# Optimization experiments

Hardware: AMD Instinct MI355X
Metric: run time of the kernel (lower is better)

Reference implementation:

```python
import jax, jax.numpy as jnp
import numpy as np

B, S, T1, V = 32, 60, 60, 50000   # batch, post len, response len (decoder runs T1-1 steps), vocab
E, A, H, ATT, DI = 300, 300, 512, 512, 512  # word emb, affect emb, rnn hidden, attention size, decoder input


def setup_inputs() -> dict:
    key = jax.random.key(0)
    ks = jax.random.split(key, 20)
    p = lambda i, shape: jax.random.normal(ks[i], shape, jnp.float32) * 0.02
    z = lambda n: jnp.zeros((n,), jnp.float32)
    return {
        'posts': jax.random.randint(ks[0], (B, S), 0, V),
        'responses': jax.random.randint(ks[1], (B, T1), 0, V),
        'len_posts': jnp.full((B,), S, jnp.int32),
        'emb': p(2, (V, E)), 'affect_emb': p(3, (V, A)),
        'enc_Wi': p(4, (3 * H, E)), 'enc_Wh': p(5, (3 * H, H)), 'enc_bi': z(3 * H), 'enc_bh': z(3 * H),
        'aff_Wi': p(6, (3 * H, A)), 'aff_Wh': p(7, (3 * H, H)), 'aff_bi': z(3 * H), 'aff_bh': z(3 * H),
        'Wp': p(8, (H, 2 * H)), 'bp': z(H),
        'Wl': p(9, (DI, E + H + ATT)), 'bl': z(DI),
        'dec_Wi': p(10, (3 * H, DI)), 'dec_Wh': p(11, (3 * H, H)), 'dec_bi': z(3 * H), 'dec_bh': z(3 * H),
        'Wa': p(12, (H, H)), 'Wc': p(13, (ATT, H)), 'bc': z(ATT),
        'Wv': p(14, (V, H + ATT)), 'bv': z(V),
    }


def _gru_cell(x, h, Wi, Wh, bi, bh):
    gi = x @ Wi.T + bi
    gh = h @ Wh.T + bh
    ir, iz, inn = jnp.split(gi, 3, -1)
    hr, hz, hn = jnp.split(gh, 3, -1)
    r = jax.nn.sigmoid(ir + hr)
    zg = jax.nn.sigmoid(iz + hz)
    n = jnp.tanh(inn + r * hn)
    return (1.0 - zg) * n + zg * h


def _gru_seq(xs, h0, Wi, Wh, bi, bh):
    # xs: [S, B, in] -> (outputs [S,B,H], h_last [B,H])
    def step(h, x):
        h2 = _gru_cell(x, h, Wi, Wh, bi, bh)
        return h2, h2
    hT, ys = jax.lax.scan(step, h0, xs)
    return ys, hT


def reference(posts, responses, len_posts, emb, affect_emb,
              enc_Wi, enc_Wh, enc_bi, enc_bh,
              aff_Wi, aff_Wh, aff_bi, aff_bh,
              Wp, bp, Wl, bl,
              dec_Wi, dec_Wh, dec_bi, dec_bh,
              Wa, Wc, bc, Wv, bv):
    embed_posts = emb[posts]            # [B,S,E]
    affect_posts = affect_emb[posts]    # [B,S,A]
    h0 = jnp.zeros((posts.shape[0], H), embed_posts.dtype)

    _, state_encoder = _gru_seq(embed_posts.transpose(1, 0, 2), h0, enc_Wi, enc_Wh, enc_bi, enc_bh)
    out_affect, state_affect = _gru_seq(affect_posts.transpose(1, 0, 2), h0, aff_Wi, aff_Wh, aff_bi, aff_bh)
    context_affect = out_affect[-1]     # [B,H] (all lengths == S)
    K = out_affect.transpose(1, 0, 2)   # [B,S,H] attention keys/values

    # PrepareState: Linear + tanh on concat of both encoder final states
    state0 = jnp.tanh(jnp.concatenate([state_encoder, state_affect], -1) @ Wp.T + bp)

    dec_in = emb[responses[:, :-1]].transpose(1, 0, 2)  # [T,B,E]
    init_attn = jnp.zeros((posts.shape[0], ATT), embed_posts.dtype)

    def dec_step(carry, x_emb):
        h, attn = carry
        x = jnp.concatenate([x_emb, context_affect, attn], -1) @ Wl.T + bl
        h = _gru_cell(x, h, dec_Wi, dec_Wh, dec_bi, dec_bh)
        scores = jnp.einsum('bd,bsd->bs', h @ Wa, K)        # Luong 'general'
        w = jax.nn.softmax(scores, -1)
        ctx = jnp.einsum('bs,bsd->bd', w, K)
        attn = jnp.tanh(ctx @ Wc.T + bc)
        return (h, attn), (jnp.concatenate([h, attn], -1), w)

    _, (outs, weights) = jax.lax.scan(dec_step, (state0, init_attn), dec_in)
    outs = outs.transpose(1, 0, 2)          # [B,T,H+ATT]
    weights = weights.transpose(1, 0, 2)    # [B,T,S]
    output_vocab = jax.nn.softmax(outs @ Wv.T + bv, -1)  # [B,T,V]
    return output_vocab, weights
```

## Files before the change

### kernel.cpp

```cpp
#include <hip/hip_runtime.h>

typedef unsigned int uint32;
typedef unsigned short u16;
typedef unsigned long long u64;
typedef __attribute__((ext_vector_type(8))) short bf8;
typedef __attribute__((ext_vector_type(4))) float f4;
typedef __attribute__((ext_vector_type(4))) uint32 u32x4;

#define DEV static __device__ __forceinline__

DEV f4 MFMA(bf8 a, bf8 b, f4 c) {
  return __builtin_amdgcn_mfma_f32_16x16x32_bf16(a, b, c, 0, 0, 0);
}
DEV u16 f2bf(float f) {
  uint32 u = __float_as_uint(f);
  return (u16)((u + 0x7FFFu + ((u >> 16) & 1u)) >> 16);
}
DEV float bf2f(u16 h) { return __uint_as_float(((uint32)h) << 16); }
DEV float bfLO(uint32 u) { return __uint_as_float(u << 16); }
DEV float bfHI(uint32 u) { return __uint_as_float(u & 0xFFFF0000u); }
DEV float sigmoid_(float x) { return 1.f / (1.f + __expf(-x)); }
DEV float tanh_(float x) {
  float cx = fminf(fmaxf(x, -15.f), 15.f);
  float e = __expf(2.f * cx);
  return (e - 1.f) / (e + 1.f);
}

DEV u64 ldA64(const void* p) {
  return __hip_atomic_load((u64*)p, __ATOMIC_RELAXED, __HIP_MEMORY_SCOPE_AGENT);
}
DEV void stA64(void* p, u64 v) {
  __hip_atomic_store((u64*)p, v, __ATOMIC_RELAXED, __HIP_MEMORY_SCOPE_AGENT);
}
DEV void stA32(int* p, int v) {
  __hip_atomic_store(p, v, __ATOMIC_RELAXED, __HIP_MEMORY_SCOPE_AGENT);
}
DEV bf8 pk_frag(u64 lo, u64 hi) {
  u32x4 v = {(uint32)lo, (uint32)(lo >> 32), (uint32)hi, (uint32)(hi >> 32)};
  return __builtin_bit_cast(bf8, v);
}

DEV void wait_vm0() { asm volatile("s_waitcnt vmcnt(0)" ::: "memory"); }
DEV void wait_slots(const int* slots, int n, int tgt) {
  const int lane = threadIdx.x & 63;
  for (int i = 0; i < (1 << 20); ++i) {
    int v = 0x7fffffff;
    if (lane < n)
      v = __hip_atomic_load((int*)(slots + lane), __ATOMIC_RELAXED,
                            __HIP_MEMORY_SCOPE_AGENT);
    if (__all(v >= tgt)) return;
    __builtin_amdgcn_s_sleep(1);
  }
}

namespace L {
constexpr size_t o_flags  = 0;
constexpr size_t o_rowsum = 4096;
constexpr size_t o_bcomb  = 11776;
constexpr size_t o_gistat = 17920;
constexpr size_t o_xbuf   = 214528;
constexpr size_t o_henc   = 345600;
constexpr size_t o_haff   = 411136;
constexpr size_t o_cat    = 476672;
constexpr size_t o_Kbuf   = 542208;
constexpr size_t o_KA     = 2508288;
constexpr size_t o_embP   = 4474368;
constexpr size_t o_embA   = 5703168;
constexpr size_t o_embD   = 6931968;
constexpr size_t o_encWi  = 8140288;
constexpr size_t o_affWi  = 9123328;
constexpr size_t o_Whe    = 10106368;
constexpr size_t o_Wha    = 11679232;
constexpr size_t o_decWi  = 13252096;
constexpr size_t o_WlT    = 14824960;
constexpr size_t o_Wa     = 16184832;
constexpr size_t o_Wp     = 16709120;
constexpr size_t o_wq     = 17757696;
constexpr size_t o_Wcomb  = 18281984;
constexpr size_t o_WdE    = 26441216;
constexpr size_t o_WdA    = 27424256;
constexpr size_t o_Wd2    = 28997120;
constexpr size_t o_giE    = 32142848;
constexpr size_t o_giA    = 43939328;
constexpr size_t o_giD    = 55735808;
constexpr size_t o_outsB  = 67335680;
constexpr size_t o_WvB    = 71267840;
constexpr size_t WS_FULL  = 174028288;
constexpr size_t WOFF = 94400000;
}

__global__ __launch_bounds__(256) void kp_gather(
    const int* __restrict__ posts, const int* __restrict__ resp,
    const float* __restrict__ emb, const float* __restrict__ aemb, char* ws)
{
  using namespace L;
  const int gid = blockIdx.x * 256 + threadIdx.x;
  const int r = gid / 320, e = gid - r * 320;
  u16* embP = (u16*)(ws + o_embP);
// ... 33 lines not shown
  gid -= 983040;
  if (gid < 2359296) {
    const int g = (int)(gid / 786432);
    const long u = gid - (long)g * 786432;
    const float* src = g == 0 ? encWh : (g == 1 ? affWh : dWi);
    u16* dst = (u16*)(ws + (g == 0 ? o_Whe : (g == 1 ? o_Wha : o_decWi)));
    dst[u] = f2bf(src[u]);
    return;
  }
  gid -= 2359296;
  if (gid < 679936) {
    const int j = (int)(gid >> 9), k = (int)(gid & 511);
    ((u16*)(ws + o_WlT))[gid] = f2bf(j < 1324 ? Wl[(size_t)k * 1324 + j] : 0.f);
    return;
  }
  gid -= 679936;
  if (gid < 262144) { ((u16*)(ws + o_Wa))[gid] = f2bf(Wa[gid]); return; }
  gid -= 262144;
  if (gid < 524288) { ((u16*)(ws + o_Wp))[gid] = f2bf(Wp[gid]); return; }
  gid -= 524288;
  if (gid < 131072) {
    const int q = (int)(gid & 3), j = (int)((gid >> 2) & 511), g4 = (int)(gid >> 11);
    const int d0 = g4 * 8 + q * 2;
    const uint32 lo = f2bf(Wc[(size_t)j * 512 + d0]);
    const uint32 hi = f2bf(Wc[(size_t)j * 512 + d0 + 1]);
    ((uint32*)(ws + o_wq))[gid] = lo | (hi << 16);
    return;
  }
  gid -= 131072;
  if (gid < 2944) {
    if (gid < 1024) ((uint32*)(ws + o_flags))[gid] = 0;
    else ((uint32*)(ws + o_rowsum))[gid - 1024] = 0;
    return;
  }
  gid -= 2944;
  if (gid < 49152) {
    if (gid < 16384) ((uint32*)(ws + o_outsB + (size_t)1888 * 1024 * 2))[gid] = 0;
    else if (gid < 32768) ((uint32*)(ws + o_henc))[gid - 16384] = 0;
    else ((uint32*)(ws + o_haff))[gid - 32768] = 0;
  }
}

__global__ __launch_bounds__(256) void kp_bcomb(
    const float* __restrict__ dWi, const float* __restrict__ bl,
    const float* __restrict__ dbi, char* ws)
{
  const int i = blockIdx.x * 256 + threadIdx.x;
  if (i >= 1536) return;
  float a = dbi[i];
  for (int k = 0; k < 512; ++k) a += dWi[(size_t)i * 512 + k] * bl[k];
  ((float*)(ws + L::o_bcomb))[i] = a;
}

__global__ __launch_bounds__(256) void kp_wv(const float* __restrict__ Wv, char* ws)
{
  const long gid = (long)blockIdx.x * 256 + threadIdx.x;
  const int r = (int)(gid >> 8), q = (int)(gid & 255);
  u16* WvB = (u16*)(ws + L::o_WvB);
  uint2 o;
  if (r < 50000) {
    const float4 f = *(const float4*)(Wv + (size_t)r * 1024 + q * 4);
    o.x = (uint32)f2bf(f.x) | ((uint32)f2bf(f.y) << 16);
    o.y = (uint32)f2bf(f.z) | ((uint32)f2bf(f.w) << 16);
  } else { o.x = 0u; o.y = 0u; }
  *(uint2*)(WvB + (size_t)r * 1024 + q * 4) = o;
}

__global__ __launch_bounds__(256) void kp_pack2(
    const float* __restrict__ Wcomb, const float* __restrict__ dWh, char* ws)
{
  using namespace L;
  long gid = (long)blockIdx.x * 256 + threadIdx.x;
  if (gid < 491520) {
    const int n = (int)(gid / 320), e = (int)(gid - (long)n * 320);
    ((u16*)(ws + o_WdE))[gid] = f2bf(e < 300 ? Wcomb[(size_t)n * 1328 + e] : 0.f);
    return;
  }
  gid -= 491520;
  if (gid < 786432) {
    const int n = (int)(gid >> 9), k = (int)(gid & 511);
    ((u16*)(ws + o_WdA))[gid] = f2bf(Wcomb[(size_t)n * 1328 + 300 + k]);
    return;
  }
  gid -= 786432;
  if (gid < 1572864) {
    const int n = (int)(gid >> 10), k = (int)(gid & 1023);
    const float v = (k < 512) ? Wcomb[(size_t)n * 1328 + 812 + k]
                              : dWh[(size_t)n * 512 + (k - 512)];
    ((u16*)(ws + o_Wd2))[gid] = f2bf(v);
  }
}

__global__ __launch_bounds__(256) void k_gemm_nt(
    const u16* __restrict__ A, const u16* __restrict__ Bm,
    float* __restrict__ C, const float* __restrict__ bias,
    const int M, const int N, const int Kp)
{
  const int mt = blockIdx.x, cb = blockIdx.y;
  const int w = threadIdx.x >> 6, lane = threadIdx.x & 63;
  const int l15 = lane & 15, lhi = lane >> 4;
  const u16* arow = A + (size_t)(mt * 16 + l15) * Kp + lhi * 8;
  const int c0 = cb * 256 + w * 64;
  f4 acc[4];
#pragma unroll
  for (int nn = 0; nn < 4; ++nn) acc[nn] = (f4){0.f, 0.f, 0.f, 0.f};
  for (int k = 0; k < Kp; k += 32) {
    const bf8 a = *(const bf8*)(arow + k);
#pragma unroll
    for (int nn = 0; nn < 4; ++nn) {
      const int cs = c0 + nn * 16;
      if (cs < N) {
        const bf8 b = *(const bf8*)(Bm + (size_t)(cs + l15) * Kp + k + lhi * 8);
        acc[nn] = MFMA(a, b, acc[nn]);
      }
    }
  }
#pragma unroll
  for (int nn = 0; nn < 4; ++nn) {
    const int cs = c0 + nn * 16;
    if (cs >= N) continue;
    const int c = cs + l15;
    const float bb = bias ? bias[c] : 0.f;
#pragma unroll
    for (int j = 0; j < 4; ++j) {
      const int r = mt * 16 + lhi * 4 + j;
      C[(size_t)r * N + c] = acc[nn][j] + bb;
    }
  }
}

__global__ __launch_bounds__(256, 1) void k_enc(
    char* __restrict__ ws, const float* __restrict__ enc_bh,
    const float* __restrict__ aff_bh)
{
  using namespace L;
  const int tid = threadIdx.x, blk = blockIdx.x;
  const int wave = tid >> 6, lane = tid & 63;
  const int l15 = lane & 15, lhi = lane >> 4;
  const int g = blk >> 5;
  const bool act = wave < 2;
  int* flags = (int*)(ws + o_flags);
  int* slotE = flags + 128 + g * 64;
  const u16* Wh = (const u16*)(ws + (g ? o_Wha : o_Whe));
  const float* gi = (const float*)(ws + (g ? o_giA : o_giE));
  const float* bh = g ? aff_bh : enc_bh;
  u16* hbuf = (u16*)(ws + (g ? o_haff : o_henc));
  u16* cat = (u16*)(ws + o_cat);
  u16* Kb = (u16*)(ws + o_Kbuf);

  const int wid = (blk & 31) * 2 + (wave & 1);
  const int btile = wid >> 5, ctile = wid & 31;
  const int bl = btile * 16 + l15;
  const int c0 = ctile * 16 + lhi * 4;
  const u16* wr0 = Wh + (size_t)(ctile * 16 + l15) * 512 + lhi * 8;
  const u16* wr1 = wr0 + (size_t)512 * 512;
  const u16* wr2 = wr1 + (size_t)512 * 512;
  f4 bhr4 = {0.f, 0.f, 0.f, 0.f}, bhz4 = bhr4, bhn4 = bhr4;
  if (act) {
    bhr4 = *(const f4*)(bh + c0);
    bhz4 = *(const f4*)(bh + 512 + c0);
    bhn4 = *(const f4*)(bh + 1024 + c0);
  }
  for (int s = 0; s < 60; ++s) {
    const u16* hin = hbuf + (s & 1) * (32 * 512);
    u16* hout = hbuf + ((s & 1) ^ 1) * (32 * 512);
    if (act) {
      const u16* brow = hin + bl * 512 + lhi * 8;
      u64 flo[16], fhi[16];
#pragma unroll
      for (int kk = 0; kk < 16; ++kk) {
        flo[kk] = ldA64(brow + kk * 32);
        fhi[kk] = ldA64(brow + kk * 32 + 4);
      }
      const u64 hq = ldA64(hin + bl * 512 + c0);
      f4 ar = {0.f, 0.f, 0.f, 0.f}, az = ar, an = ar;
#pragma unroll
      for (int kk = 0; kk < 16; ++kk) {
        const bf8 hf = pk_frag(flo[kk], fhi[kk]);
        ar = MFMA(*(const bf8*)(wr0 + kk * 32), hf, ar);
        az = MFMA(*(const bf8*)(wr1 + kk * 32), hf, az);
        an = MFMA(*(const bf8*)(wr2 + kk * 32), hf, an);
      }
      const float* gr = gi + (size_t)(s * 32 + bl) * 1536;
      const f4 g0 = *(const f4*)(gr + c0);
      const f4 g1 = *(const f4*)(gr + 512 + c0);
      const f4 g2 = *(const f4*)(gr + 1024 + c0);
      u64 pk = 0;
#pragma unroll
      for (int j = 0; j < 4; ++j) {
        const float r = sigmoid_(g0[j] + ar[j] + bhr4[j]);
        const float z = sigmoid_(g1[j] + az[j] + bhz4[j]);
        const float n = tanh_(g2[j] + r * (an[j] + bhn4[j]));
        const float hold = bf2f((u16)(hq >> (16 * j)));
        pk |= (u64)f2bf((1.f - z) * n + z * hold) << (16 * j);
      }
      stA64(hout + bl * 512 + c0, pk);
      if (g) *(u64*)(Kb + (size_t)(s * 32 + bl) * 512 + c0) = pk;
      if (s == 59) *(u64*)(cat + bl * 1024 + g * 512 + c0) = pk;
    }
    wait_vm0();
    __syncthreads();
    if (tid == 0) stA32(&slotE[blk & 31], s + 1);
    if (wave == 2) wait_slots(slotE, 32, s + 1);
    __syncthreads();
  }
}

__global__ __launch_bounds__(256) void k_mid(char* __restrict__ ws,
                                             const float* __restrict__ bp)
{
  using namespace L;
  const int tid = threadIdx.x, blk = blockIdx.x;
  const int wave = tid >> 6, lane = tid & 63;
  const int l15 = lane & 15, lhi = lane >> 4;
  u16* xb = (u16*)(ws + o_xbuf);
  u16* cat = (u16*)(ws + o_cat);
  u16* Kb = (u16*)(ws + o_Kbuf);

  if (blk < 16) {
    const u16* Wp_ = (const u16*)(ws + o_Wp);
    const int wid = blk * 4 + wave;
    const int btile = wid >> 5, ctile = wid & 31;
    const int bl = btile * 16 + l15;
    const int c0 = ctile * 16 + lhi * 4;
    const u16* arow = Wp_ + (size_t)(ctile * 16 + l15) * 1024 + lhi * 8;
    const u16* brow = cat + bl * 1024 + lhi * 8;
    f4 acc = {0.f, 0.f, 0.f, 0.f};
    for (int k = 0; k < 1024; k += 32)
      acc = MFMA(*(const bf8*)(arow + k), *(const bf8*)(brow + k), acc);
    const f4 bp4 = *(const f4*)(bp + c0);
    u64 pk = 0;
#pragma unroll
    for (int j = 0; j < 4; ++j)
      pk |= (u64)f2bf(tanh_(acc[j] + bp4[j])) << (16 * j);
    *(u64*)(xb + bl * 1024 + 512 + c0) = pk;
    *(u64*)(xb + bl * 1024 + c0) = 0;
  } else if (blk < 32) {
    const u16* WdA = (const u16*)(ws + o_WdA);
    const float* bco = (const float*)(ws + o_bcomb);
    float* gst = (float*)(ws + o_gistat);
    const int wid = (blk - 16) * 4 + wave;
    const int btile = wid >> 5, ctb = wid & 31;
    const int bl = btile * 16 + l15;
    const int c0 = ctb * 16 + lhi * 4;
    const u16* brow = cat + bl * 1024 + 512 + lhi * 8;
    const u16* a0p = WdA + (size_t)(ctb * 16 + l15) * 512 + lhi * 8;
    const u16* a1p = a0p + (size_t)512 * 512;
    const u16* a2p = a1p + (size_t)512 * 512;
    f4 a0 = {0.f, 0.f, 0.f, 0.f}, a1 = a0, a2 = a0;
    for (int k = 0; k < 512; k += 32) {
      const bf8 bfr = *(const bf8*)(brow + k);
      a0 = MFMA(*(const bf8*)(a0p + k), bfr, a0);
      a1 = MFMA(*(const bf8*)(a1p + k), bfr, a1);
      a2 = MFMA(*(const bf8*)(a2p + k), bfr, a2);
    }
    const f4 v0 = *(const f4*)(bco + c0);
    const f4 v1 = *(const f4*)(bco + 512 + c0);
    const f4 v2 = *(const f4*)(bco + 1024 + c0);
    *(f4*)(gst + bl * 1536 + c0) = a0 + v0;
    *(f4*)(gst + bl * 1536 + 512 + c0) = a1 + v1;
    *(f4*)(gst + bl * 1536 + 1024 + c0) = a2 + v2;
  } else {
    const u16* Wa_ = (const u16*)(ws + o_Wa);
    u16* KAp = (u16*)(ws + o_KA);
    const int widK = (blk - 32) * 4 + wave;
    for (int task = widK; task < 3840; task += 192) {
      const int mt = task >> 5, ct = task & 31;
      const int m = mt * 16 + l15;
      const int c0 = ct * 16 + lhi * 4;
      const u16* arow = Wa_ + (size_t)(ct * 16 + l15) * 512 + lhi * 8;
      const u16* brow = Kb + (size_t)m * 512 + lhi * 8;
      f4 acc = {0.f, 0.f, 0.f, 0.f};
      for (int k = 0; k < 512; k += 32)
        acc = MFMA(*(const bf8*)(arow + k), *(const bf8*)(brow + k), acc);
      u64 pk = 0;
#pragma unroll
      for (int j = 0; j < 4; ++j) pk |= (u64)f2bf(acc[j]) << (16 * j);
      *(u64*)(KAp + (size_t)m * 512 + c0) = pk;
    }
  }
}

__global__ __launch_bounds__(256, 1) void k_dec(
    char* __restrict__ ws, float* __restrict__ out,
    const float* __restrict__ dec_bh, const float* __restrict__ bc)
{
  using namespace L;
  const int tid = threadIdx.x, blk = blockIdx.x;
  const int wave = tid >> 6, lane = tid & 63;
  const int l15 = lane & 15, lhi = lane >> 4;
  int* flags = (int*)(ws + o_flags);
  int* slotA = flags;
  int* slotB = flags + 64;

  __shared__ float hsm[512];
  __shared__ float ctxs[512];
  __shared__ float scb[64];
  __shared__ float wsb[64];
  __shared__ u16 attn_sm[256];

  u16* xb = (u16*)(ws + o_xbuf);
  u16* outs = (u16*)(ws + o_outsB);

  if (blk < 32) {
    const bool act = wave < 2;
    const u16* Wd2 = (const u16*)(ws + o_Wd2);
    const float* gst = (const float*)(ws + o_gistat);
    const float* gD = (const float*)(ws + o_giD);
    const int wid = (blk & 31) * 2 + (wave & 1);
    const int btile = wid >> 5, ctile = wid & 31;
    const int bl = btile * 16 + l15;
    const int c0 = ctile * 16 + lhi * 4;
    const u16* wr = Wd2 + (size_t)(ctile * 16 + l15) * 1024 + lhi * 8;
    const u16* wz = wr + (size_t)512 * 1024;
    const u16* wn = wz + (size_t)512 * 1024;
    f4 bhr4 = {0.f, 0.f, 0.f, 0.f}, bhz4 = bhr4, bhn4 = bhr4;
    f4 s0 = bhr4, s1 = bhr4, s2 = bhr4;
    if (act) {
      bhr4 = *(const f4*)(dec_bh + c0);
      bhz4 = *(const f4*)(dec_bh + 512 + c0);
      bhn4 = *(const f4*)(dec_bh + 1024 + c0);
      s0 = *(const f4*)(gst + bl * 1536 + c0);
      s1 = *(const f4*)(gst + bl * 1536 + 512 + c0);
      s2 = *(const f4*)(gst + bl * 1536 + 1024 + c0);
    }
    for (int t = 0; t < 59; ++t) {
      const u16* xin = xb + (t & 1) * (32 * 1024);
      u16* xout = xb + ((t & 1) ^ 1) * (32 * 1024);
      const u16* brow = xin + bl * 1024 + lhi * 8;
      f4 ar = {0.f, 0.f, 0.f, 0.f}, az = ar, anx = ar, anh = ar;
      u64 hq = 0;
      f4 d0 = ar, d1 = ar, d2 = ar;
      if (t) {
        if (wave == 2) wait_slots(slotA, 32, t);
        __syncthreads();
      }
      if (act) {
        u64 flo[16], fhi[16];
#pragma unroll
        for (int kk = 0; kk < 16; ++kk) {
          flo[kk] = ldA64(brow + (16 + kk) * 32);
          fhi[kk] = ldA64(brow + (16 + kk) * 32 + 4);
        }
        hq = ldA64(xin + bl * 1024 + 512 + c0);
        const float* g2p = gD + (size_t)(t * 32 + bl) * 1536;
        d0 = *(const f4*)(g2p + c0);
        d1 = *(const f4*)(g2p + 512 + c0);
        d2 = *(const f4*)(g2p + 1024 + c0);
#pragma unroll
        for (int kk = 0; kk < 16; ++kk) {
          const bf8 xf = pk_frag(flo[kk], fhi[kk]);
          ar = MFMA(*(const bf8*)(wr + (16 + kk) * 32), xf, ar);
          az = MFMA(*(const bf8*)(wz + (16 + kk) * 32), xf, az);
          anh = MFMA(*(const bf8*)(wn + (16 + kk) * 32), xf, anh);
        }
      }
      if (t) {
        if (wave == 2) wait_slots(slotB, 64, t);
        __syncthreads();
      }
      if (act) {
        u64 glo[16], ghi[16];
#pragma unroll
        for (int kk = 0; kk < 16; ++kk) {
          glo[kk] = ldA64(brow + kk * 32);
          ghi[kk] = ldA64(brow + kk * 32 + 4);
        }
#pragma unroll
        for (int kk = 0; kk < 16; ++kk) {
          const bf8 xf = pk_frag(glo[kk], ghi[kk]);
          ar = MFMA(*(const bf8*)(wr + kk * 32), xf, ar);
          az = MFMA(*(const bf8*)(wz + kk * 32), xf, az);
          anx = MFMA(*(const bf8*)(wn + kk * 32), xf, anx);
        }
        u64 pk = 0;
#pragma unroll
        for (int j = 0; j < 4; ++j) {
          const float r = sigmoid_(s0[j] + d0[j] + ar[j] + bhr4[j]);
          const float z = sigmoid_(s1[j] + d1[j] + az[j] + bhz4[j]);
          const float n = tanh_(s2[j] + d2[j] + anx[j] + r * (anh[j] + bhn4[j]));
          const float hold = bf2f((u16)(hq >> (16 * j)));
          pk |= (u64)f2bf((1.f - z) * n + z * hold) << (16 * j);
        }
        stA64(xout + bl * 1024 + 512 + c0, pk);
        *(u64*)(outs + (size_t)(bl * 59 + t) * 1024 + c0) = pk;
      }
      wait_vm0();
      __syncthreads();
      if (tid == 0) stA32(&slotA[blk], t + 1);
    }
  } else {
    const int idx = blk - 32;
    const int b = idx >> 1, half = idx & 1;
    const u16* KAp = (const u16*)(ws + o_KA);
    const u16* Kb = (const u16*)(ws + o_Kbuf);
    const uint4* wq = (const uint4*)(ws + o_wq);
    for (int t = 0; t < 59; ++t) {
      if (wave == 0) wait_slots(slotA, 32, t + 1);
      __syncthreads();
      const u16* xcur = xb + ((t & 1) ^ 1) * (32 * 1024);
      if (tid < 128) {
        const u64 hv = ldA64(xcur + b * 1024 + 512 + tid * 4);
        const uint32 w0 = (uint32)hv, w1 = (uint32)(hv >> 32);
        hsm[tid * 4 + 0] = bfLO(w0);
        hsm[tid * 4 + 1] = bfHI(w0);
        hsm[tid * 4 + 2] = bfLO(w1);
        hsm[tid * 4 + 3] = bfHI(w1);
      }
      __syncthreads();
      if (tid < 240) {
        const int s = tid >> 2, q = tid & 3;
        const u16* kr = KAp + (size_t)(s * 32 + b) * 512 + q * 128;
        const float* hq = &hsm[q * 128];
        float acc0 = 0.f, acc1 = 0.f;
#pragma unroll 4
        for (int i = 0; i < 128; i += 8) {
          const uint2 k4 = *(const uint2*)(kr + i);
          const uint2 k5 = *(const uint2*)(kr + i + 4);
          const float4 h4 = *(const float4*)(hq + i);
          const float4 h5 = *(const float4*)(hq + i + 4);
          acc0 += h4.x * bfLO(k4.x) + h4.y * bfHI(k4.x)
                + h4.z * bfLO(k4.y) + h4.w * bfHI(k4.y);
          acc1 += h5.x * bfLO(k5.x) + h5.y * bfHI(k5.x)
                + h5.z * bfLO(k5.y) + h5.w * bfHI(k5.y);
        }
        float acc = acc0 + acc1;
        acc += __shfl_xor(acc, 1);
        acc += __shfl_xor(acc, 2);
        if ((tid & 3) == 0) scb[s] = acc;
      }
      __syncthreads();
      if (tid < 64) {
        const float v = (tid < 60) ? scb[tid] : -1e30f;
        float m = v;
#pragma unroll
        for (int d = 1; d < 64; d <<= 1) m = fmaxf(m, __shfl_xor(m, d));
        const float e = (tid < 60) ? __expf(v - m) : 0.f;
        float sm = e;
#pragma unroll
        for (int d = 1; d < 64; d <<= 1) sm += __shfl_xor(sm, d);
        const float w = e / sm;
        if (tid < 60) {
          wsb[tid] = w;
          if (half == 0) out[WOFF + (size_t)(b * 59 + t) * 60 + tid] = w;
        }
      }
      __syncthreads();
      {
        float c0a = 0.f, c0b = 0.f, c1a = 0.f, c1b = 0.f;
#pragma unroll 2
        for (int s = 0; s < 60; s += 2) {
          const float w0 = wsb[s], w1 = wsb[s + 1];
          const u16* kr0 = Kb + (size_t)(s * 32 + b) * 512;
          const u16* kr1 = Kb + (size_t)((s + 1) * 32 + b) * 512;
          c0a += w0 * bf2f(kr0[tid]);
          c1a += w0 * bf2f(kr0[tid + 256]);
          c0b += w1 * bf2f(kr1[tid]);
          c1b += w1 * bf2f(kr1[tid + 256]);
        }
        ctxs[tid] = c0a + c0b;
        ctxs[tid + 256] = c1a + c1b;
      }
      __syncthreads();
      const int jj = half * 256 + tid;
      float faa[4] = {0.f, 0.f, 0.f, 0.f};
      float fbb[4] = {0.f, 0.f, 0.f, 0.f};
#pragma unroll 4
      for (int g4 = 0; g4 < 64; ++g4) {
        const uint4 wv4 = wq[g4 * 512 + jj];
        const float4 ca = *(const float4*)&ctxs[g4 * 8];
        const float4 cb2 = *(const float4*)&ctxs[g4 * 8 + 4];
        faa[g4 & 3] += ca.x * bfLO(wv4.x) + ca.y * bfHI(wv4.x)
                     + ca.z * bfLO(wv4.y) + ca.w * bfHI(wv4.y);
        fbb[g4 & 3] += cb2.x * bfLO(wv4.z) + cb2.y * bfHI(wv4.z)
                     + cb2.z * bfLO(wv4.w) + cb2.w * bfHI(wv4.w);
      }
      const float fa = bc[jj] + faa[0] + faa[1] + faa[2] + faa[3]
                     + fbb[0] + fbb[1] + fbb[2] + fbb[3];
      attn_sm[tid] = f2bf(tanh_(fa));
      __syncthreads();
      if (tid < 64) {
        u16* xout = xb + ((t & 1) ^ 1) * (32 * 1024);
        const u64 pk = (u64)attn_sm[tid * 4] | ((u64)attn_sm[tid * 4 + 1] << 16)
                     | ((u64)attn_sm[tid * 4 + 2] << 32) | ((u64)attn_sm[tid * 4 + 3] << 48);
        const int cc = half * 256 + tid * 4;
        stA64(xout + b * 1024 + cc, pk);
        *(u64*)(outs + (size_t)(b * 59 + t) * 1024 + 512 + cc) = pk;
      }
      wait_vm0();
      __syncthreads();
      if (tid == 0) stA32(&slotB[idx], t + 1);
    }
  }
}

__global__ __launch_bounds__(512, 2) void k_vocab2(
    const u16* __restrict__ A, const u16* __restrict__ Bm,
    const float* __restrict__ bvv, float* __restrict__ out,
    float* __restrict__ rowsum)
{
  __shared__ u16 As[2][128][40];
  __shared__ u16 Bs[2][256][40];
  const int tid = threadIdx.x;
  const int bid = blockIdx.x;
  const int xcd = bid & 7, sub = bid >> 3;
  const int wgid = (xcd < 4 ? xcd * 368 : 4 * 368 + (xcd - 4) * 367) + sub;
  const int mtile = wgid % 15, ntile = wgid / 15;
  const int rbase = mtile * 128, cbase = ntile * 256;

  const int wave = tid >> 6, lane = tid & 63;
  const int l15 = lane & 15, lhi = lane >> 4;
  const int m0 = (wave >> 2) * 64, n0 = (wave & 3) * 64;

  const int sar = tid >> 2, sak = (tid & 3) * 8;
  const u16* gA = A + (size_t)(rbase + sar) * 1024 + sak;
  const u16* gB0 = Bm + (size_t)(cbase + sar) * 1024 + sak;
  const u16* gB1 = Bm + (size_t)(cbase + 128 + sar) * 1024 + sak;

  f4 acc[4][4];
#pragma unroll
  for (int mi = 0; mi < 4; ++mi)
#pragma unroll
    for (int ni = 0; ni < 4; ++ni) acc[mi][ni] = (f4){0.f, 0.f, 0.f, 0.f};

  uint4 ra, rb0, rb1;
  ra = *(const uint4*)(gA);
  rb0 = *(const uint4*)(gB0);
  rb1 = *(const uint4*)(gB1);
  *(uint4*)&As[0][sar][sak] = ra;
  *(uint4*)&Bs[0][sar][sak] = rb0;
  *(uint4*)&Bs[0][128 + sar][sak] = rb1;
  __syncthreads();

  int cur = 0;
#pragma unroll 1
  for (int t = 0; t < 32; ++t) {
    if (t < 31) {
      const int k0 = (t + 1) * 32;
      ra = *(const uint4*)(gA + k0);
      rb0 = *(const uint4*)(gB0 + k0);
      rb1 = *(const uint4*)(gB1 + k0);
    }
    bf8 af[4], bfr[4];
#pragma unroll
    for (int mi = 0; mi < 4; ++mi)
      af[mi] = *(const bf8*)&As[cur][m0 + mi * 16 + l15][lhi * 8];
#pragma unroll
    for (int ni = 0; ni < 4; ++ni)
      bfr[ni] = *(const bf8*)&Bs[cur][n0 + ni * 16 + l15][lhi * 8];
#pragma unroll
    for (int mi = 0; mi < 4; ++mi)
#pragma unroll
      for (int ni = 0; ni < 4; ++ni)
        acc[mi][ni] = MFMA(af[mi], bfr[ni], acc[mi][ni]);
    if (t < 31) {
      __syncthreads();
      *(uint4*)&As[cur ^ 1][sar][sak] = ra;
      *(uint4*)&Bs[cur ^ 1][sar][sak] = rb0;
      *(uint4*)&Bs[cur ^ 1][128 + sar][sak] = rb1;
      __syncthreads();
      cur ^= 1;
    }
  }

#pragma unroll
  for (int mi = 0; mi < 4; ++mi) {
    float rs[4] = {0.f, 0.f, 0.f, 0.f};
#pragma unroll
    for (int ni = 0; ni < 4; ++ni) {
      const int c = cbase + n0 + ni * 16 + l15;
      if (c < 50000) {
        const float bb = bvv[c];
#pragma unroll
        for (int j = 0; j < 4; ++j) {
          const int r = rbase + m0 + mi * 16 + lhi * 4 + j;
          if (r < 1888) {
            const float e = __expf(acc[mi][ni][j] + bb);
            out[(size_t)r * 50000 + c] = e;
            rs[j] += e;
          }
        }
      }
    }
#pragma unroll
    for (int j = 0; j < 4; ++j) {
#pragma unroll
      for (int d = 1; d < 16; d <<= 1) rs[j] += __shfl_xor(rs[j], d);
    }
    if (l15 == 0) {
#pragma unroll
      for (int j = 0; j < 4; ++j) {
        const int r = rbase + m0 + mi * 16 + lhi * 4 + j;
        if (r < 1888) atomicAdd(&rowsum[r], rs[j]);
      }
    }
  }
}

__global__ __launch_bounds__(512) void k_vocab0(
    const u16* __restrict__ A, const float* __restrict__ WvF,
    const float* __restrict__ bv, float* __restrict__ out,
    float* __restrict__ rowsum)
{
  const int bid = blockIdx.x;
  const int x = bid & 7, jj = bid >> 3;
  const int mtile = jj % 15, nseq = jj / 15;
  const int ntile = nseq * 8 + x;
  if (ntile >= 196) return;
  const int w = threadIdx.x >> 6, lane = threadIdx.x & 63;
  const int l15 = lane & 15, lhi = lane >> 4;
  const int rbase = mtile * 128 + w * 16;
  const u16* arow = A + (size_t)(rbase + l15) * 1024 + lhi * 8;
  const int cbase = ntile * 256;
  f4 acc[16];
#pragma unroll
  for (int nn = 0; nn < 16; ++nn) acc[nn] = (f4){0.f, 0.f, 0.f, 0.f};
  for (int k = 0; k < 1024; k += 32) {
    const bf8 a = *(const bf8*)(arow + k);
#pragma unroll
    for (int nn = 0; nn < 16; ++nn) {
      const int cs = cbase + nn * 16;
      bf8 bfr = {0, 0, 0, 0, 0, 0, 0, 0};
      if (cs < 50000) {
        const float* p = WvF + (size_t)(cs + l15) * 1024 + k + lhi * 8;
        const float4 f0 = *(const float4*)p;
        const float4 f1 = *(const float4*)(p + 4);
        bfr[0] = (short)(__float_as_uint(f0.x) >> 16);
        bfr[1] = (short)(__float_as_uint(f0.y) >> 16);
        bfr[2] = (short)(__float_as_uint(f0.z) >> 16);
        bfr[3] = (short)(__float_as_uint(f0.w) >> 16);
        bfr[4] = (short)(__float_as_uint(f1.x) >> 16);
        bfr[5] = (short)(__float_as_uint(f1.y) >> 16);
        bfr[6] = (short)(__float_as_uint(f1.z) >> 16);
        bfr[7] = (short)(__float_as_uint(f1.w) >> 16);
      }
      acc[nn] = MFMA(a, bfr, acc[nn]);
    }
  }
  float rsv[4] = {0.f, 0.f, 0.f, 0.f};
#pragma unroll
  for (int nn = 0; nn < 16; ++nn) {
    const int cs = cbase + nn * 16;
    if (cs >= 50000) continue;
    const int c = cs + l15;
    const float bb = bv[c];
#pragma unroll
    for (int j = 0; j < 4; ++j) {
      const int r = rbase + lhi * 4 + j;
      if (r < 1888) {
        const float e = __expf(acc[nn][j] + bb);
        out[(size_t)r * 50000 + c] = e;
        rsv[j] += e;
      }
    }
  }
#pragma unroll
  for (int j = 0; j < 4; ++j) {
#pragma unroll
    for (int d = 1; d < 16; d <<= 1) rsv[j] += __shfl_xor(rsv[j], d);
  }
  if (l15 == 0) {
#pragma unroll
    for (int j = 0; j < 4; ++j) {
      const int r = rbase + lhi * 4 + j;
      if (r < 1888) atomicAdd(&rowsum[r], rsv[j]);
    }
  }
}

__global__ void k_invrow(float* rs)
{
  const int i = blockIdx.x * 256 + threadIdx.x;
  if (i < 1920) {
    const float s = rs[i];
    rs[i] = (s > 0.f) ? 1.f / s : 0.f;
  }
}

__global__ __launch_bounds__(256) void k_scale(float* __restrict__ out,
                                               const float* __restrict__ inv)
{
  const int bid = blockIdx.x;
  const int r = bid / 49, ch = bid - r * 49;
  const int c = ch * 1024 + threadIdx.x * 4;
  if (c < 50000) {
    const float s = inv[r];
    float4* p = (float4*)(out + (size_t)r * 50000 + c);
    float4 v = *p;
    v.x *= s; v.y *= s; v.z *= s; v.w *= s;
    *p = v;
  }
}

extern "C" void kernel_launch(void* const* d_in, const int* in_sizes, int n_in,
                              void* d_out, int out_size, void* d_ws, size_t ws_size,
                              hipStream_t stream) {
  const int* posts = (const int*)d_in[0];
  const int* resp = (const int*)d_in[1];
  const float* emb = (const float*)d_in[3];
  const float* aemb = (const float*)d_in[4];
  const float* encWi = (const float*)d_in[5];
  const float* encWh = (const float*)d_in[6];
  const float* enc_bi = (const float*)d_in[7];
  const float* enc_bh = (const float*)d_in[8];
  const float* affWi = (const float*)d_in[9];
  const float* affWh = (const float*)d_in[10];
  const float* aff_bi = (const float*)d_in[11];
  const float* aff_bh = (const float*)d_in[12];
  const float* Wp = (const float*)d_in[13];
  const float* bp = (const float*)d_in[14];
  const float* Wl = (const float*)d_in[15];
  const float* bl = (const float*)d_in[16];
  const float* dWi = (const float*)d_in[17];
  const float* dWh = (const float*)d_in[18];
  const float* dbi = (const float*)d_in[19];
  const float* dbh = (const float*)d_in[20];
  const float* Wa = (const float*)d_in[21];
  const float* Wc = (const float*)d_in[22];
  const float* bc = (const float*)d_in[23];
  const float* Wv = (const float*)d_in[24];
  const float* bv = (const float*)d_in[25];
  char* ws = (char*)d_ws;
  float* out = (float*)d_out;
  const bool useWvB = ws_size >= L::WS_FULL;

  kp_gather<<<4760, 256, 0, stream>>>(posts, resp, emb, aemb, ws);
  kp_wconv<<<19500, 256, 0, stream>>>(encWi, affWi, encWh, affWh, dWi, Wl, Wa, Wp, Wc, ws);
  kp_bcomb<<<6, 256, 0, stream>>>(dWi, bl, dbi, ws);
  if (useWvB) kp_wv<<<50176, 256, 0, stream>>>(Wv, ws);

  k_gemm_nt<<<dim3(96, 6), 256, 0, stream>>>(
      (const u16*)(ws + L::o_decWi), (const u16*)(ws + L::o_WlT),
      (float*)(ws + L::o_Wcomb), nullptr, 1536, 1328, 512);
  kp_pack2<<<11136, 256, 0, stream>>>((const float*)(ws + L::o_Wcomb), dWh, ws);

  k_gemm_nt<<<dim3(120, 6), 256, 0, stream>>>(
      (const u16*)(ws + L::o_embP), (const u16*)(ws + L::o_encWi),
      (float*)(ws + L::o_giE), enc_bi, 1920, 1536, 320);
  k_gemm_nt<<<dim3(120, 6), 256, 0, stream>>>(
      (const u16*)(ws + L::o_embA), (const u16*)(ws + L::o_affWi),
      (float*)(ws + L::o_giA), aff_bi, 1920, 1536, 320);
  k_gemm_nt<<<dim3(118, 6), 256, 0, stream>>>(
      (const u16*)(ws + L::o_embD), (const u16*)(ws + L::o_WdE),
      (float*)(ws + L::o_giD), nullptr, 1888, 1536, 320);

  k_enc<<<64, 256, 0, stream>>>(ws, enc_bh, aff_bh);
  k_mid<<<80, 256, 0, stream>>>(ws, bp);
  k_dec<<<96, 256, 0, stream>>>(ws, out, dbh, bc);

  if (useWvB)
    k_vocab2<<<2940, 512, 0, stream>>>(
        (const u16*)(ws + L::o_outsB), (const u16*)(ws + L::o_WvB),
        bv, out, (float*)(ws + L::o_rowsum));
  else
    k_vocab0<<<2944, 512, 0, stream>>>(
        (const u16*)(ws + L::o_outsB), Wv, bv, out, (float*)(ws + L::o_rowsum));

  k_invrow<<<8, 256, 0, stream>>>((float*)(ws + L::o_rowsum));
  k_scale<<<92512, 256, 0, stream>>>(out, (const float*)(ws + L::o_rowsum));
}
```

Baseline: 2.574 ms.

## Overlap serial encoder/decoder recurrences with independent GEMM and vocab work

Folds the decoder input GEMM and the Wv bf16 conversion into extra blocks of the encoder kernel, so they run on idle CUs during the serial encoder recurrence. The vocab projection becomes extra blocks of the decoder kernel. Each vocab tile spin-waits on decoder step flags and starts as soon as its rows are ready. To support this, the decoder output buffer is laid out time-major with atomic stores, and the vocab epilogues remap rows back to batch-major. This hides the latency-bound recurrences behind throughput work. The risks are spin-wait deadlock if the persistent recurrence blocks are not scheduled, and contention that slows the critical path.

```diff
diff --git a/kernel.cpp b/kernel.cpp
--- a/kernel.cpp
+++ b/kernel.cpp
@@ -43,7 +43,7 @@
 DEV void wait_vm0() { asm volatile("s_waitcnt vmcnt(0)" ::: "memory"); }
 DEV void wait_slots(const int* slots, int n, int tgt) {
   const int lane = threadIdx.x & 63;
-  for (int i = 0; i < (1 << 20); ++i) {
+  for (int i = 0; i < (1 << 21); ++i) {
     int v = 0x7fffffff;
     if (lane < n)
       v = __hip_atomic_load((int*)(slots + lane), __ATOMIC_RELAXED,
@@ -183,20 +183,6 @@
   ((float*)(ws + L::o_bcomb))[i] = a;
 }
 
-__global__ __launch_bounds__(256) void kp_wv(const float* __restrict__ Wv, char* ws)
-{
-  const long gid = (long)blockIdx.x * 256 + threadIdx.x;
-  const int r = (int)(gid >> 8), q = (int)(gid & 255);
-  u16* WvB = (u16*)(ws + L::o_WvB);
-  uint2 o;
-  if (r < 50000) {
-    const float4 f = *(const float4*)(Wv + (size_t)r * 1024 + q * 4);
-    o.x = (uint32)f2bf(f.x) | ((uint32)f2bf(f.y) << 16);
-    o.y = (uint32)f2bf(f.z) | ((uint32)f2bf(f.w) << 16);
-  } else { o.x = 0u; o.y = 0u; }
-  *(uint2*)(WvB + (size_t)r * 1024 + q * 4) = o;
-}
-
 __global__ __launch_bounds__(256) void kp_pack2(
     const float* __restrict__ Wcomb, const float* __restrict__ dWh, char* ws)
 {
@@ -260,80 +246,122 @@
   }
 }
 
-__global__ __launch_bounds__(256, 1) void k_enc(
+__global__ __launch_bounds__(256) void k_encplus(
     char* __restrict__ ws, const float* __restrict__ enc_bh,
-    const float* __restrict__ aff_bh)
+    const float* __restrict__ aff_bh, const float* __restrict__ Wv)
 {
   using namespace L;
   const int tid = threadIdx.x, blk = blockIdx.x;
   const int wave = tid >> 6, lane = tid & 63;
   const int l15 = lane & 15, lhi = lane >> 4;
-  const int g = blk >> 5;
-  const bool act = wave < 2;
-  int* flags = (int*)(ws + o_flags);
-  int* slotE = flags + 128 + g * 64;
-  const u16* Wh = (const u16*)(ws + (g ? o_Wha : o_Whe));
-  const float* gi = (const float*)(ws + (g ? o_giA : o_giE));
-  const float* bh = g ? aff_bh : enc_bh;
-  u16* hbuf = (u16*)(ws + (g ? o_haff : o_henc));
-  u16* cat = (u16*)(ws + o_cat);
-  u16* Kb = (u16*)(ws + o_Kbuf);
-
-  const int wid = (blk & 31) * 2 + (wave & 1);
-  const int btile = wid >> 5, ctile = wid & 31;
-  const int bl = btile * 16 + l15;
-  const int c0 = ctile * 16 + lhi * 4;
-  const u16* wr0 = Wh + (size_t)(ctile * 16 + l15) * 512 + lhi * 8;
-  const u16* wr1 = wr0 + (size_t)512 * 512;
-  const u16* wr2 = wr1 + (size_t)512 * 512;
-  f4 bhr4 = {0.f, 0.f, 0.f, 0.f}, bhz4 = bhr4, bhn4 = bhr4;
-  if (act) {
-    bhr4 = *(const f4*)(bh + c0);
-    bhz4 = *(const f4*)(bh + 512 + c0);
-    bhn4 = *(const f4*)(bh + 1024 + c0);
-  }
-  for (int s = 0; s < 60; ++s) {
-    const u16* hin = hbuf + (s & 1) * (32 * 512);
-    u16* hout = hbuf + ((s & 1) ^ 1) * (32 * 512);
+
+  if (blk < 64) {
+    const int g = blk >> 5;
+    const bool act = wave < 2;
+    int* flags = (int*)(ws + o_flags);
+    int* slotE = flags + 128 + g * 64;
+    const u16* Wh = (const u16*)(ws + (g ? o_Wha : o_Whe));
+    const float* gi = (const float*)(ws + (g ? o_giA : o_giE));
+    const float* bh = g ? aff_bh : enc_bh;
+    u16* hbuf = (u16*)(ws + (g ? o_haff : o_henc));
+    u16* cat = (u16*)(ws + o_cat);
+    u16* Kb = (u16*)(ws + o_Kbuf);
+
+    const int wid = (blk & 31) * 2 + (wave & 1);
+    const int btile = wid >> 5, ctile = wid & 31;
+    const int bl = btile * 16 + l15;
+    const int c0 = ctile * 16 + lhi * 4;
+    const u16* wr0 = Wh + (size_t)(ctile * 16 + l15) * 512 + lhi * 8;
+    const u16* wr1 = wr0 + (size_t)512 * 512;
+    const u16* wr2 = wr1 + (size_t)512 * 512;
+    f4 bhr4 = {0.f, 0.f, 0.f, 0.f}, bhz4 = bhr4, bhn4 = bhr4;
     if (act) {
-      const u16* brow = hin + bl * 512 + lhi * 8;
-      u64 flo[16], fhi[16];
-#pragma unroll
-      for (int kk = 0; kk < 16; ++kk) {
-        flo[kk] = ldA64(brow + kk * 32);
-        fhi[kk] = ldA64(brow + kk * 32 + 4);
-      }
-      const u64 hq = ldA64(hin + bl * 512 + c0);
-      f4 ar = {0.f, 0.f, 0.f, 0.f}, az = ar, an = ar;
-#pragma unroll
-      for (int kk = 0; kk < 16; ++kk) {
-        const bf8 hf = pk_frag(flo[kk], fhi[kk]);
-        ar = MFMA(*(const bf8*)(wr0 + kk * 32), hf, ar);
-        az = MFMA(*(const bf8*)(wr1 + kk * 32), hf, az);
-        an = MFMA(*(const bf8*)(wr2 + kk * 32), hf, an);
-      }
-      const float* gr = gi + (size_t)(s * 32 + bl) * 1536;
-      const f4 g0 = *(const f4*)(gr + c0);
-      const f4 g1 = *(const f4*)(gr + 512 + c0);
-      const f4 g2 = *(const f4*)(gr + 1024 + c0);
-      u64 pk = 0;
-#pragma unroll
-      for (int j = 0; j < 4; ++j) {
-        const float r = sigmoid_(g0[j] + ar[j] + bhr4[j]);
-        const float z = sigmoid_(g1[j] + az[j] + bhz4[j]);
-        const float n = tanh_(g2[j] + r * (an[j] + bhn4[j]));
-        const float hold = bf2f((u16)(hq >> (16 * j)));
-        pk |= (u64)f2bf((1.f - z) * n + z * hold) << (16 * j);
-      }
-      stA64(hout + bl * 512 + c0, pk);
-      if (g) *(u64*)(Kb + (size_t)(s * 32 + bl) * 512 + c0) = pk;
-      if (s == 59) *(u64*)(cat + bl * 1024 + g * 512 + c0) = pk;
-    }
-    wait_vm0();
-    __syncthreads();
-    if (tid == 0) stA32(&slotE[blk & 31], s + 1);
-    if (wave == 2) wait_slots(slotE, 32, s + 1);
-    __syncthreads();
+      bhr4 = *(const f4*)(bh + c0);
+      bhz4 = *(const f4*)(bh + 512 + c0);
+      bhn4 = *(const f4*)(bh + 1024 + c0);
+    }
+    for (int s = 0; s < 60; ++s) {
+      const u16* hin = hbuf + (s & 1) * (32 * 512);
+      u16* hout = hbuf + ((s & 1) ^ 1) * (32 * 512);
+      if (act) {
+        const u16* brow = hin + bl * 512 + lhi * 8;
+        u64 flo[16], fhi[16];
+#pragma unroll
+        for (int kk = 0; kk < 16; ++kk) {
+          flo[kk] = ldA64(brow + kk * 32);
+          fhi[kk] = ldA64(brow + kk * 32 + 4);
+        }
+        const u64 hq = ldA64(hin + bl * 512 + c0);
+        f4 ar = {0.f, 0.f, 0.f, 0.f}, az = ar, an = ar;
+#pragma unroll
+        for (int kk = 0; kk < 16; ++kk) {
+          const bf8 hf = pk_frag(flo[kk], fhi[kk]);
+          ar = MFMA(*(const bf8*)(wr0 + kk * 32), hf, ar);
+          az = MFMA(*(const bf8*)(wr1 + kk * 32), hf, az);
+          an = MFMA(*(const bf8*)(wr2 + kk * 32), hf, an);
+        }
+        const float* gr = gi + (size_t)(s * 32 + bl) * 1536;
+        const f4 g0 = *(const f4*)(gr + c0);
+        const f4 g1 = *(const f4*)(gr + 512 + c0);
+        const f4 g2 = *(const f4*)(gr + 1024 + c0);
+        u64 pk = 0;
+#pragma unroll
+        for (int j = 0; j < 4; ++j) {
+          const float r = sigmoid_(g0[j] + ar[j] + bhr4[j]);
+          const float z = sigmoid_(g1[j] + az[j] + bhz4[j]);
+          const float n = tanh_(g2[j] + r * (an[j] + bhn4[j]));
+          const float hold = bf2f((u16)(hq >> (16 * j)));
+          pk |= (u64)f2bf((1.f - z) * n + z * hold) << (16 * j);
+        }
+        stA64(hout + bl * 512 + c0, pk);
+        if (g) *(u64*)(Kb + (size_t)(s * 32 + bl) * 512 + c0) = pk;
+        if (s == 59) *(u64*)(cat + bl * 1024 + g * 512 + c0) = pk;
+      }
+      wait_vm0();
+      __syncthreads();
+      if (tid == 0) stA32(&slotE[blk & 31], s + 1);
+      if (wave == 2) wait_slots(slotE, 32, s + 1);
+      __syncthreads();
+    }
+  } else if (blk < 772) {
+    const int bb = blk - 64;
+    const int mt = bb % 118, cb = bb / 118;
+    const u16* A = (const u16*)(ws + o_embD);
+    const u16* Bm = (const u16*)(ws + o_WdE);
+    float* C = (float*)(ws + o_giD);
+    const int Kp = 320, N = 1536;
+    const int w = wave;
+    const u16* arow = A + (size_t)(mt * 16 + l15) * Kp + lhi * 8;
+    const int c0 = cb * 256 + w * 64;
+    f4 acc[4];
+#pragma unroll
+    for (int nn = 0; nn < 4; ++nn) acc[nn] = (f4){0.f, 0.f, 0.f, 0.f};
+    for (int k = 0; k < Kp; k += 32) {
+      const bf8 a = *(const bf8*)(arow + k);
+#pragma unroll
+      for (int nn = 0; nn < 4; ++nn) {
+        const bf8 b = *(const bf8*)(Bm + (size_t)(c0 + nn * 16 + l15) * Kp + k + lhi * 8);
+        acc[nn] = MFMA(a, b, acc[nn]);
+      }
+    }
+#pragma unroll
+    for (int nn = 0; nn < 4; ++nn) {
+      const int c = c0 + nn * 16 + l15;
+#pragma unroll
+      for (int j = 0; j < 4; ++j)
+        C[(size_t)(mt * 16 + lhi * 4 + j) * N + c] = acc[nn][j];
+    }
+  } else {
+    const long gid = (long)(blk - 772) * 256 + tid;
+    const int r = (int)(gid >> 8), q = (int)(gid & 255);
+    u16* WvB = (u16*)(ws + o_WvB);
+    uint2 o;
+    if (r < 50000) {
+      const float4 f = *(const float4*)(Wv + (size_t)r * 1024 + q * 4);
+      o.x = (uint32)f2bf(f.x) | ((uint32)f2bf(f.y) << 16);
+      o.y = (uint32)f2bf(f.z) | ((uint32)f2bf(f.w) << 16);
+    } else { o.x = 0u; o.y = 0u; }
+    if (r < 50176) *(uint2*)(WvB + (size_t)r * 1024 + q * 4) = o;
   }
 }
 
@@ -412,9 +440,10 @@
   }
 }
 
-__global__ __launch_bounds__(256, 1) void k_dec(
+__global__ __launch_bounds__(256, 1) void k_decvoc(
     char* __restrict__ ws, float* __restrict__ out,
-    const float* __restrict__ dec_bh, const float* __restrict__ bc)
+    const float* __restrict__ dec_bh, const float* __restrict__ bc,
+    const float* __restrict__ bv)
 {
   using namespace L;
   const int tid = threadIdx.x, blk = blockIdx.x;
@@ -429,6 +458,8 @@
   __shared__ float scb[64];
   __shared__ float wsb[64];
   __shared__ u16 attn_sm[256];
+  __shared__ u16 vAs[2][128][40];
+  __shared__ u16 vBs[2][128][40];
 
   u16* xb = (u16*)(ws + o_xbuf);
   u16* outs = (u16*)(ws + o_outsB);
@@ -514,13 +545,13 @@
           pk |= (u64)f2bf((1.f - z) * n + z * hold) << (16 * j);
         }
         stA64(xout + bl * 1024 + 512 + c0, pk);
-        *(u64*)(outs + (size_t)(bl * 59 + t) * 1024 + c0) = pk;
+        stA64(outs + (size_t)(t * 32 + bl) * 1024 + c0, pk);
       }
       wait_vm0();
       __syncthreads();
       if (tid == 0) stA32(&slotA[blk], t + 1);
     }
-  } else {
+  } else if (blk < 96) {
     const int idx = blk - 32;
     const int b = idx >> 1, half = idx & 1;
     const u16* KAp = (const u16*)(ws + o_KA);
@@ -616,113 +647,116 @@
                      | ((u64)attn_sm[tid * 4 + 2] << 32) | ((u64)attn_sm[tid * 4 + 3] << 48);
         const int cc = half * 256 + tid * 4;
         stA64(xout + b * 1024 + cc, pk);
-        *(u64*)(outs + (size_t)(b * 59 + t) * 1024 + 512 + cc) = pk;
+        stA64(outs + (size_t)(t * 32 + b) * 1024 + 512 + cc, pk);
       }
       wait_vm0();
       __syncthreads();
       if (tid == 0) stA32(&slotB[idx], t + 1);
     }
-  }
-}
-
-__global__ __launch_bounds__(512, 2) void k_vocab2(
-    const u16* __restrict__ A, const u16* __restrict__ Bm,
-    const float* __restrict__ bvv, float* __restrict__ out,
-    float* __restrict__ rowsum)
-{
-  __shared__ u16 As[2][128][40];
-  __shared__ u16 Bs[2][256][40];
-  const int tid = threadIdx.x;
-  const int bid = blockIdx.x;
-  const int xcd = bid & 7, sub = bid >> 3;
-  const int wgid = (xcd < 4 ? xcd * 368 : 4 * 368 + (xcd - 4) * 367) + sub;
-  const int mtile = wgid % 15, ntile = wgid / 15;
-  const int rbase = mtile * 128, cbase = ntile * 256;
-
-  const int wave = tid >> 6, lane = tid & 63;
-  const int l15 = lane & 15, lhi = lane >> 4;
-  const int m0 = (wave >> 2) * 64, n0 = (wave & 3) * 64;
-
-  const int sar = tid >> 2, sak = (tid & 3) * 8;
-  const u16* gA = A + (size_t)(rbase + sar) * 1024 + sak;
-  const u16* gB0 = Bm + (size_t)(cbase + sar) * 1024 + sak;
-  const u16* gB1 = Bm + (size_t)(cbase + 128 + sar) * 1024 + sak;
-
-  f4 acc[4][4];
-#pragma unroll
-  for (int mi = 0; mi < 4; ++mi)
-#pragma unroll
-    for (int ni = 0; ni < 4; ++ni) acc[mi][ni] = (f4){0.f, 0.f, 0.f, 0.f};
-
-  uint4 ra, rb0, rb1;
-  ra = *(const uint4*)(gA);
-  rb0 = *(const uint4*)(gB0);
-  rb1 = *(const uint4*)(gB1);
-  *(uint4*)&As[0][sar][sak] = ra;
-  *(uint4*)&Bs[0][sar][sak] = rb0;
-  *(uint4*)&Bs[0][128 + sar][sak] = rb1;
-  __syncthreads();
-
-  int cur = 0;
+  } else {
+    const int vb = blk - 96;
+    const int mtile = vb / 392, ntile = vb % 392;
+    const int rbase = mtile * 128, cbase = ntile * 128;
+    const int tgt = (4 * mtile + 4 < 59) ? (4 * mtile + 4) : 59;
+    if (wave == 0) {
+      wait_slots(slotB, 64, tgt);
+      __builtin_amdgcn_fence(__ATOMIC_ACQUIRE, "agent");
+    }
+    __syncthreads();
+
+    const u16* A = outs;
+    const u16* Bm = (const u16*)(ws + o_WvB);
+    float* rowsum = (float*)(ws + o_rowsum);
+    const int m0 = (wave >> 1) * 64, n0 = (wave & 1) * 64;
+    const int sr0 = tid >> 2, sk = (tid & 3) * 8;
+
+    f4 acc[4][4];
+#pragma unroll
+    for (int mi = 0; mi < 4; ++mi)
+#pragma unroll
+      for (int ni = 0; ni < 4; ++ni) acc[mi][ni] = (f4){0.f, 0.f, 0.f, 0.f};
+
+    const u16* gA0 = A + (size_t)(rbase + sr0) * 1024 + sk;
+    const u16* gA1 = A + (size_t)(rbase + 64 + sr0) * 1024 + sk;
+    const u16* gB0 = Bm + (size_t)(cbase + sr0) * 1024 + sk;
+    const u16* gB1 = Bm + (size_t)(cbase + 64 + sr0) * 1024 + sk;
+
+    uint4 a0 = *(const uint4*)(gA0), a1 = *(const uint4*)(gA1);
+    uint4 b0 = *(const uint4*)(gB0), b1 = *(const uint4*)(gB1);
+    *(uint4*)&vAs[0][sr0][sk] = a0;
+    *(uint4*)&vAs[0][64 + sr0][sk] = a1;
+    *(uint4*)&vBs[0][sr0][sk] = b0;
+    *(uint4*)&vBs[0][64 + sr0][sk] = b1;
+    __syncthreads();
+
+    int cur = 0;
 #pragma unroll 1
-  for (int t = 0; t < 32; ++t) {
-    if (t < 31) {
-      const int k0 = (t + 1) * 32;
-      ra = *(const uint4*)(gA + k0);
-      rb0 = *(const uint4*)(gB0 + k0);
-      rb1 = *(const uint4*)(gB1 + k0);
-    }
-    bf8 af[4], bfr[4];
-#pragma unroll
-    for (int mi = 0; mi < 4; ++mi)
-      af[mi] = *(const bf8*)&As[cur][m0 + mi * 16 + l15][lhi * 8];
-#pragma unroll
-    for (int ni = 0; ni < 4; ++ni)
-      bfr[ni] = *(const bf8*)&Bs[cur][n0 + ni * 16 + l15][lhi * 8];
-#pragma unroll
-    for (int mi = 0; mi < 4; ++mi)
+    for (int kt = 0; kt < 32; ++kt) {
+      if (kt < 31) {
+        const int k0 = (kt + 1) * 32;
+        a0 = *(const uint4*)(gA0 + k0);
+        a1 = *(const uint4*)(gA1 + k0);
+        b0 = *(const uint4*)(gB0 + k0);
+        b1 = *(const uint4*)(gB1 + k0);
+      }
+      bf8 af[4], bfr[4];
+#pragma unroll
+      for (int mi = 0; mi < 4; ++mi)
+        af[mi] = *(const bf8*)&vAs[cur][m0 + mi * 16 + l15][lhi * 8];
 #pragma unroll
       for (int ni = 0; ni < 4; ++ni)
-        acc[mi][ni] = MFMA(af[mi], bfr[ni], acc[mi][ni]);
-    if (t < 31) {
-      __syncthreads();
-      *(uint4*)&As[cur ^ 1][sar][sak] = ra;
-      *(uint4*)&Bs[cur ^ 1][sar][sak] = rb0;
-      *(uint4*)&Bs[cur ^ 1][128 + sar][sak] = rb1;
-      __syncthreads();
-      cur ^= 1;
-    }
-  }
-
-#pragma unroll
-  for (int mi = 0; mi < 4; ++mi) {
-    float rs[4] = {0.f, 0.f, 0.f, 0.f};
-#pragma unroll
-    for (int ni = 0; ni < 4; ++ni) {
-      const int c = cbase + n0 + ni * 16 + l15;
-      if (c < 50000) {
-        const float bb = bvv[c];
-#pragma unroll
-        for (int j = 0; j < 4; ++j) {
-          const int r = rbase + m0 + mi * 16 + lhi * 4 + j;
-          if (r < 1888) {
-            const float e = __expf(acc[mi][ni][j] + bb);
-            out[(size_t)r * 50000 + c] = e;
-            rs[j] += e;
-          }
-        }
-      }
-    }
-#pragma unroll
-    for (int j = 0; j < 4; ++j) {
-#pragma unroll
-      for (int d = 1; d < 16; d <<= 1) rs[j] += __shfl_xor(rs[j], d);
-    }
-    if (l15 == 0) {
+        bfr[ni] = *(const bf8*)&vBs[cur][n0 + ni * 16 + l15][lhi * 8];
+#pragma unroll
+      for (int mi = 0; mi < 4; ++mi)
+#pragma unroll
+        for (int ni = 0; ni < 4; ++ni)
+          acc[mi][ni] = MFMA(af[mi], bfr[ni], acc[mi][ni]);
+      if (kt < 31) {
+        __syncthreads();
+        *(uint4*)&vAs[cur ^ 1][sr0][sk] = a0;
+        *(uint4*)&vAs[cur ^ 1][64 + sr0][sk] = a1;
+        *(uint4*)&vBs[cur ^ 1][sr0][sk] = b0;
+        *(uint4*)&vBs[cur ^ 1][64 + sr0][sk] = b1;
+        __syncthreads();
+        cur ^= 1;
+      }
+    }
+
+#pragma unroll
+    for (int mi = 0; mi < 4; ++mi) {
+      float rs[4] = {0.f, 0.f, 0.f, 0.f};
+      int ro_[4]; bool rv[4];
 #pragma unroll
       for (int j = 0; j < 4; ++j) {
         const int r = rbase + m0 + mi * 16 + lhi * 4 + j;
-        if (r < 1888) atomicAdd(&rowsum[r], rs[j]);
+        const int tt = r >> 5, bb2 = r & 31;
+        rv[j] = tt < 59;
+        ro_[j] = bb2 * 59 + tt;
+      }
+#pragma unroll
+      for (int ni = 0; ni < 4; ++ni) {
+        const int c = cbase + n0 + ni * 16 + l15;
+        if (c < 50000) {
+          const float bb = bv[c];
+#pragma unroll
+          for (int j = 0; j < 4; ++j) {
+            if (rv[j]) {
+              const float e = __expf(acc[mi][ni][j] + bb);
+              out[(size_t)ro_[j] * 50000 + c] = e;
+              rs[j] += e;
+            }
+          }
+        }
+      }
+#pragma unroll
+      for (int j = 0; j < 4; ++j) {
+#pragma unroll
+        for (int d = 1; d < 16; d <<= 1) rs[j] += __shfl_xor(rs[j], d);
+      }
+      if (l15 == 0) {
+#pragma unroll
+        for (int j = 0; j < 4; ++j)
+          if (rv[j]) atomicAdd(&rowsum[ro_[j]], rs[j]);
       }
     }
   }
@@ -768,34 +802,25 @@
       acc[nn] = MFMA(a, bfr, acc[nn]);
     }
   }
-  float rsv[4] = {0.f, 0.f, 0.f, 0.f};
-#pragma unroll
-  for (int nn = 0; nn < 16; ++nn) {
-    const int cs = cbase + nn * 16;
-    if (cs >= 50000) continue;
-    const int c = cs + l15;
-    const float bb = bv[c];
-#pragma unroll
-    for (int j = 0; j < 4; ++j) {
-      const int r = rbase + lhi * 4 + j;
-      if (r < 1888) {
-        const float e = __expf(acc[nn][j] + bb);
-        out[(size_t)r * 50000 + c] = e;
-        rsv[j] += e;
-      }
-    }
-  }
 #pragma unroll
   for (int j = 0; j < 4; ++j) {
-#pragma unroll
-    for (int d = 1; d < 16; d <<= 1) rsv[j] += __shfl_xor(rsv[j], d);
-  }
-  if (l15 == 0) {
-#pragma unroll
-    for (int j = 0; j < 4; ++j) {
-      const int r = rbase + lhi * 4 + j;
-      if (r < 1888) atomicAdd(&rowsum[r], rsv[j]);
-    }
+    const int r = rbase + lhi * 4 + j;
+    const int tt = r >> 5, bb2 = r & 31;
+    if (tt >= 59) continue;
+    const int ro = bb2 * 59 + tt;
+    float rsv = 0.f;
+#pragma unroll
+    for (int nn = 0; nn < 16; ++nn) {
+      const int cs = cbase + nn * 16;
+      if (cs >= 50000) continue;
+      const int c = cs + l15;
+      const float e = __expf(acc[nn][j] + bv[c]);
+      out[(size_t)ro * 50000 + c] = e;
+      rsv += e;
+    }
+#pragma unroll
+    for (int d = 1; d < 16; d <<= 1) rsv += __shfl_xor(rsv, d);
+    if (l15 == 0) atomicAdd(&rowsum[ro], rsv);
   }
 }
 
@@ -858,7 +883,6 @@
   kp_gather<<<4760, 256, 0, stream>>>(posts, resp, emb, aemb, ws);
   kp_wconv<<<19500, 256, 0, stream>>>(encWi, affWi, encWh, affWh, dWi, Wl, Wa, Wp, Wc, ws);
   kp_bcomb<<<6, 256, 0, stream>>>(dWi, bl, dbi, ws);
-  if (useWvB) kp_wv<<<50176, 256, 0, stream>>>(Wv, ws);
 
   k_gemm_nt<<<dim3(96, 6), 256, 0, stream>>>(
       (const u16*)(ws + L::o_decWi), (const u16*)(ws + L::o_WlT),
@@ -871,19 +895,13 @@
   k_gemm_nt<<<dim3(120, 6), 256, 0, stream>>>(
       (const u16*)(ws + L::o_embA), (const u16*)(ws + L::o_affWi),
       (float*)(ws + L::o_giA), aff_bi, 1920, 1536, 320);
-  k_gemm_nt<<<dim3(118, 6), 256, 0, stream>>>(
-      (const u16*)(ws + L::o_embD), (const u16*)(ws + L::o_WdE),
-      (float*)(ws + L::o_giD), nullptr, 1888, 1536, 320);
-
-  k_enc<<<64, 256, 0, stream>>>(ws, enc_bh, aff_bh);
+
+  k_encplus<<<useWvB ? 50948 : 772, 256, 0, stream>>>(ws, enc_bh, aff_bh, Wv);
   k_mid<<<80, 256, 0, stream>>>(ws, bp);
-  k_dec<<<96, 256, 0, stream>>>(ws, out, dbh, bc);
-
-  if (useWvB)
-    k_vocab2<<<2940, 512, 0, stream>>>(
-        (const u16*)(ws + L::o_outsB), (const u16*)(ws + L::o_WvB),
-        bv, out, (float*)(ws + L::o_rowsum));
-  else
+
+  k_decvoc<<<useWvB ? 5976 : 96, 256, 0, stream>>>(ws, out, dbh, bc, bv);
+
+  if (!useWvB)
     k_vocab0<<<2944, 512, 0, stream>>>(
         (const u16*)(ws + L::o_outsB), Wv, bv, out, (float*)(ws + L::o_rowsum));
 
```

After: 2.859 ms. 11.1% more time.
